# Optimization experiments

Measured on AMD Instinct MI355X. Metric: run time of the kernel, lower is better.

## Reference

```python
import jax, jax.numpy as jnp
import numpy as np

B, M = 1024, 200000
D_IN, DIM, D_OUT = 256, 128, 10
T = 1.0
EPS = 1e-7


def setup_inputs() -> dict:
    key = jax.random.key(0)
    k1, k2, k3, k4, k5 = jax.random.split(key, 5)
    x = jax.random.normal(k1, (B, D_IN), dtype=jnp.float32)
    y = jax.random.randint(k2, (B,), 0, D_OUT)
    candidate_x = jax.random.normal(k3, (M, D_IN), dtype=jnp.float32)
    candidate_y = jax.random.randint(k4, (M,), 0, D_OUT)
    W_enc = jax.random.normal(k5, (DIM, D_IN), dtype=jnp.float32) * (1.0 / np.sqrt(D_IN))
    b_enc = jnp.zeros((DIM,), dtype=jnp.float32)
    return {"x": x, "y": y, "candidate_x": candidate_x, "candidate_y": candidate_y,
            "W_enc": W_enc, "b_enc": b_enc, "is_train": 0}


def reference(x, y, candidate_x, candidate_y, W_enc, b_enc, is_train):
    # eval path (is_train == 0): no candidate subsampling, no diagonal masking
    h = x @ W_enc.T + b_enc            # [B, DIM]
    hc = candidate_x @ W_enc.T + b_enc  # [M, DIM]
    # pairwise L2 distance (cdist, p=2)
    sq = jnp.sum(h * h, axis=-1, keepdims=True) + jnp.sum(hc * hc, axis=-1)[None, :] \
         - 2.0 * (h @ hc.T)            # [B, M]
    dist = jnp.sqrt(jnp.maximum(sq, 0.0)) / T
    p = jax.nn.softmax(-dist, axis=-1)  # [B, M]
    y1h = jax.nn.one_hot(candidate_y, D_OUT, dtype=h.dtype)  # [M, D_OUT]
    logits = p @ y1h                    # [B, D_OUT]
    return jnp.log(logits + EPS)
```

## Files before the change

kernel.cpp:

```cpp
#include <hip/hip_runtime.h>
#include <hip/hip_bf16.h>
#include <math.h>

#define B_N   1024
#define M_N   200000
#define DIN   256
#define DIMN  128
#define DOUT  10
#define EPS_F 1e-7f
#define M_PAD 200064
#define NBY   1563
#define CTILES 8
#define NGRP  ((NBY + CTILES - 1)/CTILES)
#define YPAD  200

typedef __bf16 bf16_t;
typedef __bf16 bf16x8 __attribute__((ext_vector_type(8)));
typedef float  f32x4  __attribute__((ext_vector_type(4)));


__global__ void cvt_w_kernel(const float* __restrict__ W, bf16_t* __restrict__ Wb){
    int i = blockIdx.x*256 + threadIdx.x;
    if (i < DIMN*DIN) Wb[i] = (bf16_t)W[i];
}

__global__ void hist_kernel(const int* __restrict__ cy, int* __restrict__ hist){
    __shared__ int h[DOUT];
    if (threadIdx.x < DOUT) h[threadIdx.x] = 0;
    __syncthreads();
    for (int i = blockIdx.x*blockDim.x + threadIdx.x; i < M_N; i += gridDim.x*blockDim.x)
        atomicAdd(&h[cy[i]], 1);
    __syncthreads();
    if (threadIdx.x < DOUT) atomicAdd(&hist[threadIdx.x*16], h[threadIdx.x]);
}

__global__ void prefix_kernel(const int* __restrict__ hist, int* __restrict__ cs){
    if (threadIdx.x == 0 && blockIdx.x == 0){
        int acc = 0;
        for (int c = 0; c < DOUT; ++c){ cs[c] = acc; acc += hist[c*16]; }
        cs[DOUT] = acc;
    }
}


__global__ __launch_bounds__(256) void encode_kernel(
    const float* __restrict__ src, const bf16_t* __restrict__ Wb,
    bf16_t* __restrict__ out, float* __restrict__ onorm, int N,
    const int* __restrict__ ycls, int* __restrict__ counters,
    const int* __restrict__ cs)
{
    __shared__ bf16_t As[128][136];
    __shared__ int   posL[128];
    __shared__ float nbuf[128][2];
    __shared__ int   cntL[DOUT], baseL[DOUT];
    const int tid = threadIdx.x;
    const int r0  = blockIdx.x*128;

    int myc = -1, myrank = 0;
    if (ycls != nullptr){
        if (tid < DOUT) cntL[tid] = 0;
        __syncthreads();
        if (tid < 128 && r0 + tid < N){
            myc = ycls[r0 + tid];
            myrank = atomicAdd(&cntL[myc], 1);
        }
        __syncthreads();
        if (tid < DOUT && cntL[tid] > 0)
            baseL[tid] = atomicAdd(&counters[tid*16], cntL[tid]);
        __syncthreads();
    }
    if (tid < 128)
        posL[tid] = (myc >= 0) ? (cs[myc] + baseL[myc] + myrank) : (r0 + tid);

    const int lane = tid & 63, wid = tid >> 6;
    const int wr = wid >> 1, wc = wid & 1;
    const int l15 = lane & 15, quad = lane >> 4;
    const int cbase = wc*64;

    bf16x8 ball[2][4];
    #pragma unroll
    for (int kh = 0; kh < 2; ++kh)
        #pragma unroll
        for (int ks = 0; ks < 4; ++ks){
            ball[kh][ks] = *(const bf16x8*)(Wb + (size_t)(cbase + 0*16 + l15)*DIN + kh*128 + ks*32 + quad*8);
        }

    f32x4 acc[4][4] = {};
    #pragma unroll
    for (int kh = 0; kh < 2; ++kh){
        __syncthreads();
        #pragma unroll
        for (int i = 0; i < 8; ++i){
            int idx = i*256 + tid;
            int row = idx >> 4;
            int col = (idx & 15)*8;
            int rr  = r0 + row; if (rr > N-1) rr = N-1;
            const float4* p4 = (const float4*)(src + (size_t)rr*DIN + kh*128 + col);
            float4 f0 = p4[0], f1 = p4[1];
            bf16x8 v;
            v[0]=(bf16_t)f0.x; v[1]=(bf16_t)f0.y; v[2]=(bf16_t)f0.z; v[3]=(bf16_t)f0.w;
            v[4]=(bf16_t)f1.x; v[5]=(bf16_t)f1.y; v[6]=(bf16_t)f1.z; v[7]=(bf16_t)f1.w;
            *(bf16x8*)&As[row][col] = v;
        }
        __syncthreads();
        #pragma unroll
        for (int ks = 0; ks < 4; ++ks){
            const int k  = ks*32 + quad*8;
            const int kg = kh*128 + k;
            bf16x8 a[4], b[4];
            b[0] = ball[kh][ks];
            #pragma unroll
            for (int ct = 1; ct < 4; ++ct)
                b[ct] = *(const bf16x8*)(Wb + (size_t)(cbase + ct*16 + l15)*DIN + kg);
            #pragma unroll
            for (int rt = 0; rt < 4; ++rt)
                a[rt] = *(const bf16x8*)&As[wr*64 + rt*16 + l15][k];
            #pragma unroll
            for (int rt = 0; rt < 4; ++rt)
                #pragma unroll
                for (int ct = 0; ct < 4; ++ct)
                    acc[rt][ct] = __builtin_amdgcn_mfma_f32_16x16x32_bf16(a[rt], b[ct], acc[rt][ct], 0, 0, 0);
        }
    }

    float np[4][4];
    #pragma unroll
    for (int rt = 0; rt < 4; ++rt)
        #pragma unroll
        for (int r = 0; r < 4; ++r){
            float s = 0.f;
            #pragma unroll
            for (int ct = 0; ct < 4; ++ct){ float v = acc[rt][ct][r]; s += v*v; }
            np[rt][r] = s;
        }
    #pragma unroll
    for (int m = 1; m < 16; m <<= 1)
        #pragma unroll
        for (int rt = 0; rt < 4; ++rt)
            #pragma unroll
            for (int r = 0; r < 4; ++r)
                np[rt][r] += __shfl_xor(np[rt][r], m, 64);
    if (l15 == 0){
        #pragma unroll
        for (int rt = 0; rt < 4; ++rt)
            #pragma unroll
            for (int r = 0; r < 4; ++r)
                nbuf[wr*64 + rt*16 + quad*4 + r][wc] = np[rt][r];
    }

    __syncthreads();

    #pragma unroll
    for (int rt = 0; rt < 4; ++rt)
        #pragma unroll
        for (int r = 0; r < 4; ++r){
            int rl = wr*64 + rt*16 + quad*4 + r;
            #pragma unroll
            for (int ct = 0; ct < 4; ++ct)
                As[rl][cbase + ct*16 + l15] = (bf16_t)acc[rt][ct][r];
        }
    __syncthreads();

    {
        const int rsub = tid >> 4;
        const int cpos = (tid & 15)*8;
        #pragma unroll
        for (int p = 0; p < 8; ++p){
            int rl = p*16 + rsub;
            size_t rowp = (size_t)posL[rl]*DIMN;
            *(bf16x8*)(out + rowp + cpos) = *(const bf16x8*)&As[rl][cpos];
        }
    }
    if (tid < 128){
        int rs = r0 + tid;
        if (rs < N) onorm[posL[tid]] = nbuf[tid][0] + nbuf[tid][1];
    }
}


__device__ __forceinline__ void gld_lds16(const bf16_t* g, bf16_t* l){
    __builtin_amdgcn_global_load_lds((const __attribute__((address_space(1))) void*)g,
                                     (__attribute__((address_space(3))) void*)l, 16, 0, 0);
}

__device__ __forceinline__ void bfly16(float (&s)[2][4]){
    #pragma unroll
    for (int m = 1; m < 16; m <<= 1)
        #pragma unroll
        for (int rt = 0; rt < 2; ++rt)
            #pragma unroll
            for (int r = 0; r < 4; ++r)
                s[rt][r] += __shfl_xor(s[rt][r], m, 64);
}

__device__ __forceinline__ void flushC(float (&s)[2][4], int c, int rbase,
                                       int quad, int l15, float* __restrict__ accG){
    bfly16(s);
    if (l15 == 0){
        #pragma unroll
        for (int rt = 0; rt < 2; ++rt)
            #pragma unroll
            for (int r = 0; r < 4; ++r)
                atomicAdd(&accG[(size_t)(rbase + rt*16 + quad*4 + r)*16 + c], s[rt][r]);
    }
}

__global__ __launch_bounds__(512, 4) void fused_kernel(
    const bf16_t* __restrict__ hb, const bf16_t* __restrict__ hcb,
    const float* __restrict__ hn, const float* __restrict__ hcn,
    const int* __restrict__ csg, float* __restrict__ accG)
{
    const int lin = blockIdx.y*8 + blockIdx.x;
    const int i8  = lin & 7;
    const int t   = lin >> 3;
    const int q   = t >> 3;
    const int r8  = t & 7;
    const int bx  = r8;
    const int yg  = q*8 + i8;
    if (yg >= NGRP) return;

    __shared__ bf16_t Bs0[128][128];
    __shared__ bf16_t Bs1[128][128];
    const int tid = threadIdx.x;
    const int lane = tid & 63, wid = tid >> 6;
    const int wr = wid >> 1, wc = wid & 1;
    const int l15 = lane & 15, quad = lane >> 4;
    const int rbase = bx*128 + wr*32;

    bf16x8 a[4][2];
    #pragma unroll
    for (int ks = 0; ks < 4; ++ks)
        #pragma unroll
        for (int rt = 0; rt < 2; ++rt)
            a[ks][rt] = *(const bf16x8*)(hb + (size_t)(rbase + rt*16 + l15)*DIMN + ks*32 + quad*8);

    float hnv[2][4];
    #pragma unroll
    for (int rt = 0; rt < 2; ++rt)
        #pragma unroll
        for (int r = 0; r < 4; ++r)
            hnv[rt][r] = hn[rbase + rt*16 + quad*4 + r];

    int cseg[DOUT+1];
    #pragma unroll
    for (int i = 0; i <= DOUT; ++i) cseg[i] = __builtin_amdgcn_readfirstlane(csg[i]);

    const int by0 = yg*CTILES;
    int nt = NBY - by0; if (nt > CTILES) nt = CTILES;

    float s[2][4] = {};
    int curC = -1;

    auto stage = [&](bf16_t (&Bsb)[128][128], int by){
        const int cb = by*128;
        #pragma unroll
        for (int i = 0; i < 4; ++i){
            int c   = i*512 + tid;
            int col = c >> 4, j = c & 15;
            int cc  = cb + col; if (cc > M_N-1) cc = M_N-1;
            const bf16_t* g = hcb + (size_t)cc*DIMN + ((j ^ (col & 7)) << 3);
            bf16_t* l = &Bsb[0][0] + ((i*512 + (wid << 6)) << 3);
            gld_lds16(g, l);
        }
    };

    auto compute = [&](const bf16_t (&Bsb)[128][128], int by){
        const int cbase0 = by*128;
        f32x4 acc[2][4] = {};
        const char* bsb = (const char*)&Bsb[0][0];
        #pragma unroll
        for (int ks = 0; ks < 4; ++ks){
            bf16x8 b[4];
            #pragma unroll
            for (int ct = 0; ct < 4; ++ct){
                int row = wc*64 + ct*16 + l15;
                int off = (row << 8) + ((((ks << 6) + (quad << 4))) ^ ((l15 & 7) << 4));
                b[ct] = *(const bf16x8*)(bsb + off);
            }
            #pragma unroll
            for (int rt = 0; rt < 2; ++rt)
                #pragma unroll
                for (int ct = 0; ct < 4; ++ct)
                    acc[rt][ct] = __builtin_amdgcn_mfma_f32_16x16x32_bf16(a[ks][rt], b[ct], acc[rt][ct], 0, 0, 0);
        }

        float hcnv[4];
        #pragma unroll
        for (int ct = 0; ct < 4; ++ct){
            int cc = cbase0 + wc*64 + ct*16 + l15;
            hcnv[ct] = (cc < M_N) ? hcn[cc] : 1e30f;
        }
        #pragma unroll
        for (int rt = 0; rt < 2; ++rt)
            #pragma unroll
            for (int ct = 0; ct < 4; ++ct)
                #pragma unroll
                for (int r = 0; r < 4; ++r){
                    float sq = fmaxf(fmaf(-2.0f, acc[rt][ct][r], hnv[rt][r] + hcnv[ct]), 0.0f);
                    acc[rt][ct][r] = __expf(-__builtin_amdgcn_sqrtf(sq));
                }

        const int lastc = min(cbase0 + 127, M_N - 1);
        int cLo = 0, cHi = 0;
        #pragma unroll
        for (int c = 1; c < DOUT; ++c){
            if (cbase0 >= cseg[c]) cLo = c;
            if (lastc  >= cseg[c]) cHi = c;
        }

        if (cLo == curC && cHi == curC){
            #pragma unroll
            for (int rt = 0; rt < 2; ++rt)
                #pragma unroll
                for (int r = 0; r < 4; ++r){
                    float v0 = acc[rt][0][r] + acc[rt][1][r];
                    float v1 = acc[rt][2][r] + acc[rt][3][r];
                    s[rt][r] += v0 + v1;
                }
        } else {
            if (curC >= 0) flushC(s, curC, rbase, quad, l15, accG);
            #pragma unroll
            for (int rt = 0; rt < 2; ++rt)
                #pragma unroll
                for (int r = 0; r < 4; ++r) s[rt][r] = 0.f;
            for (int c = cLo; c <= cHi; ++c){
                const int s0 = cseg[c], s1 = cseg[c+1];
                float m[2][4];
                #pragma unroll
                for (int rt = 0; rt < 2; ++rt)
                    #pragma unroll
                    for (int r = 0; r < 4; ++r){
                        float v = 0.f;
                        #pragma unroll
                        for (int ct = 0; ct < 4; ++ct){
                            int cc = cbase0 + wc*64 + ct*16 + l15;
                            v += (cc >= s0 && cc < s1) ? acc[rt][ct][r] : 0.f;
                        }
                        m[rt][r] = v;
                    }
                if (c == cHi){
                    #pragma unroll
                    for (int rt = 0; rt < 2; ++rt)
                        #pragma unroll
                        for (int r = 0; r < 4; ++r) s[rt][r] = m[rt][r];
                    curC = cHi;
                } else {
                    flushC(m, c, rbase, quad, l15, accG);
                }
            }
        }
    };

    stage(Bs0, by0);
    __syncthreads();

    #pragma unroll 1
    for (int tp = 0; tp < CTILES/2; ++tp){
        int t0 = tp*2;
        if (t0 >= nt) break;
        if (t0 + 1 < nt) stage(Bs1, by0 + t0 + 1);
        compute(Bs0, by0 + t0);
        __syncthreads();
        int t1 = t0 + 1;
        if (t1 >= nt) break;
        if (t1 + 1 < nt) stage(Bs0, by0 + t1 + 1);
        compute(Bs1, by0 + t1);
        __syncthreads();
    }
    if (curC >= 0) flushC(s, curC, rbase, quad, l15, accG);
}

__global__ void finalize_kernel(const float* __restrict__ accG, float* __restrict__ out){
    int b = blockIdx.x*blockDim.x + threadIdx.x;
    if (b < B_N){
        float v[DOUT]; float den = 0.f;
        #pragma unroll
        for (int c = 0; c < DOUT; ++c){ v[c] = accG[b*16 + c]; den += v[c]; }
        float inv = (den > 0.f) ? 1.0f/den : 0.f;
        #pragma unroll
        for (int c = 0; c < DOUT; ++c) out[b*DOUT + c] = logf(v[c]*inv + EPS_F);
    }
}


extern "C" void kernel_launch(void* const* d_in, const int* in_sizes, int n_in,
                              void* d_out, int out_size, void* d_ws, size_t ws_size,
                              hipStream_t stream)
{
    const float* x  = (const float*)d_in[0];
    const float* cx = (const float*)d_in[2];
    const int*   cy = (const int*)d_in[3];
    const float* W  = (const float*)d_in[4];
    float* out = (float*)d_out;

    char* w = (char*)d_ws;
    size_t off = 0;
    bf16_t* hcb = (bf16_t*)(w + off); off += (size_t)M_PAD*DIMN*2;
    bf16_t* hb  = (bf16_t*)(w + off); off += (size_t)B_N*DIMN*2;
    float*  hcn = (float*) (w + off); off += (size_t)M_PAD*4;
    float*  hn  = (float*) (w + off); off += (size_t)B_N*4;
    bf16_t* Wb  = (bf16_t*)(w + off); off += (size_t)DIMN*DIN*2;
    size_t zoff = off;
    float* accG = (float*)(w + off); off += (size_t)B_N*16*4;
    int* hist     = (int*)(w + off); off += 16*DOUT*4;
    int* counters = (int*)(w + off); off += 16*DOUT*4;
    int* csg      = (int*)(w + off); off += 64;
    size_t zsize = off - zoff;

    hipMemsetAsync(w + zoff, 0, zsize, stream);
    cvt_w_kernel<<<dim3((DIMN*DIN + 255)/256), dim3(256), 0, stream>>>(W, Wb);
    hist_kernel<<<dim3(256), dim3(256), 0, stream>>>(cy, hist);
    prefix_kernel<<<dim3(1), dim3(1), 0, stream>>>(hist, csg);
    encode_kernel<<<dim3(M_PAD/128), dim3(256), 0, stream>>>(cx, Wb, hcb, hcn, M_N, cy, counters, csg);
    encode_kernel<<<dim3(B_N/128), dim3(256), 0, stream>>>(x, Wb, hb, hn, B_N, nullptr, nullptr, nullptr);
    fused_kernel<<<dim3(8, YPAD), dim3(512), 0, stream>>>(hb, hcb, hn, hcn, csg, accG);
    finalize_kernel<<<dim3((B_N + 255)/256), dim3(256), 0, stream>>>(accG, out);
}
```

Baseline: 482.4 us.

## Halve candidate tile, use exp2 with prescaled norms, merge encode launches

The fused distance/softmax kernel now stages 64-column candidate tiles instead of 128, with 16 tiles per group and a higher occupancy hint. Staging uses incrementing global pointers instead of recomputing addresses. The exp(-sqrt) is rewritten as a native exp2 with norms and the dot-product factor prescaled by log2(e)^2. Per-column-half accumulators are split into separate slots to reduce atomic contention, and finalize sums the two slots. The two encode launches are merged into one grid, which removes a launch but adds branching per block.

Result: slower. 607.3 us (+25.9%).

```diff
diff --git a/kernel.cpp b/kernel.cpp
--- a/kernel.cpp
+++ b/kernel.cpp
@@ -9,14 +9,26 @@
 #define DOUT  10
 #define EPS_F 1e-7f
 #define M_PAD 200064
-#define NBY   1563
-#define CTILES 8
-#define NGRP  ((NBY + CTILES - 1)/CTILES)
+#define MBLK  1563
+#define NBY64 3126
+#define TPG   16
+#define NGRP  ((NBY64 + TPG - 1)/TPG)
 #define YPAD  200
+#define L2E2  2.0813689810056077f
 
 typedef __bf16 bf16_t;
 typedef __bf16 bf16x8 __attribute__((ext_vector_type(8)));
 typedef float  f32x4  __attribute__((ext_vector_type(4)));
+
+__device__ __forceinline__ float fast_exp2(float x){
+#if __has_builtin(__builtin_amdgcn_exp2f)
+    return __builtin_amdgcn_exp2f(x);
+#else
+    float r;
+    asm("v_exp_f32 %0, %1" : "=v"(r) : "v"(x));
+    return r;
+#endif
+}
 
 
 __global__ void cvt_w_kernel(const float* __restrict__ W, bf16_t* __restrict__ Wb){
@@ -44,9 +56,11 @@
 
 
 __global__ __launch_bounds__(256) void encode_kernel(
-    const float* __restrict__ src, const bf16_t* __restrict__ Wb,
-    bf16_t* __restrict__ out, float* __restrict__ onorm, int N,
-    const int* __restrict__ ycls, int* __restrict__ counters,
+    const float* __restrict__ cx, const float* __restrict__ xb,
+    const bf16_t* __restrict__ Wb,
+    bf16_t* __restrict__ hcb, float* __restrict__ hcn,
+    bf16_t* __restrict__ hb,  float* __restrict__ hn,
+    const int* __restrict__ cy, int* __restrict__ counters,
     const int* __restrict__ cs)
 {
     __shared__ bf16_t As[128][136];
@@ -54,7 +68,13 @@
     __shared__ float nbuf[128][2];
     __shared__ int   cntL[DOUT], baseL[DOUT];
     const int tid = threadIdx.x;
-    const int r0  = blockIdx.x*128;
+
+    const float* src; bf16_t* out; float* onorm; int N; const int* ycls; int r0;
+    if ((int)blockIdx.x < MBLK){
+        src = cx; out = hcb; onorm = hcn; N = M_N; ycls = cy; r0 = blockIdx.x*128;
+    } else {
+        src = xb; out = hb;  onorm = hn;  N = B_N; ycls = nullptr; r0 = (blockIdx.x - MBLK)*128;
+    }
 
     int myc = -1, myrank = 0;
     if (ycls != nullptr){
@@ -81,9 +101,8 @@
     #pragma unroll
     for (int kh = 0; kh < 2; ++kh)
         #pragma unroll
-        for (int ks = 0; ks < 4; ++ks){
-            ball[kh][ks] = *(const bf16x8*)(Wb + (size_t)(cbase + 0*16 + l15)*DIN + kh*128 + ks*32 + quad*8);
-        }
+        for (int ks = 0; ks < 4; ++ks)
+            ball[kh][ks] = *(const bf16x8*)(Wb + (size_t)(cbase + l15)*DIN + kh*128 + ks*32 + quad*8);
 
     f32x4 acc[4][4] = {};
     #pragma unroll
@@ -194,18 +213,18 @@
 }
 
 __device__ __forceinline__ void flushC(float (&s)[2][4], int c, int rbase,
-                                       int quad, int l15, float* __restrict__ accG){
+                                       int quad, int l15, float* __restrict__ accGp){
     bfly16(s);
     if (l15 == 0){
         #pragma unroll
         for (int rt = 0; rt < 2; ++rt)
             #pragma unroll
             for (int r = 0; r < 4; ++r)
-                atomicAdd(&accG[(size_t)(rbase + rt*16 + quad*4 + r)*16 + c], s[rt][r]);
-    }
-}
-
-__global__ __launch_bounds__(512, 4) void fused_kernel(
+                atomicAdd(&accGp[(size_t)(rbase + rt*16 + quad*4 + r)*32 + c], s[rt][r]);
+    }
+}
+
+__global__ __launch_bounds__(512, 6) void fused_kernel(
     const bf16_t* __restrict__ hb, const bf16_t* __restrict__ hcb,
     const float* __restrict__ hn, const float* __restrict__ hcn,
     const int* __restrict__ csg, float* __restrict__ accG)
@@ -219,8 +238,8 @@
     const int yg  = q*8 + i8;
     if (yg >= NGRP) return;
 
-    __shared__ bf16_t Bs0[128][128];
-    __shared__ bf16_t Bs1[128][128];
+    __shared__ bf16_t Bs0[64][128];
+    __shared__ bf16_t Bs1[64][128];
     const int tid = threadIdx.x;
     const int lane = tid & 63, wid = tid >> 6;
     const int wr = wid >> 1, wc = wid & 1;
@@ -239,68 +258,69 @@
     for (int rt = 0; rt < 2; ++rt)
         #pragma unroll
         for (int r = 0; r < 4; ++r)
-            hnv[rt][r] = hn[rbase + rt*16 + quad*4 + r];
+            hnv[rt][r] = hn[rbase + rt*16 + quad*4 + r] * L2E2;
 
     int cseg[DOUT+1];
     #pragma unroll
     for (int i = 0; i <= DOUT; ++i) cseg[i] = __builtin_amdgcn_readfirstlane(csg[i]);
 
-    const int by0 = yg*CTILES;
-    int nt = NBY - by0; if (nt > CTILES) nt = CTILES;
-
+    const int by0 = yg*TPG;
+    int nt = NBY64 - by0; if (nt > TPG) nt = TPG;
+
+    float* accGp = accG + wc*16;
     float s[2][4] = {};
     int curC = -1;
 
-    auto stage = [&](bf16_t (&Bsb)[128][128], int by){
-        const int cb = by*128;
-        #pragma unroll
-        for (int i = 0; i < 4; ++i){
-            int c   = i*512 + tid;
-            int col = c >> 4, j = c & 15;
-            int cc  = cb + col; if (cc > M_N-1) cc = M_N-1;
-            const bf16_t* g = hcb + (size_t)cc*DIMN + ((j ^ (col & 7)) << 3);
-            bf16_t* l = &Bsb[0][0] + ((i*512 + (wid << 6)) << 3);
-            gld_lds16(g, l);
-        }
+    const int c1 = 512 + tid;
+    const int col0 = tid >> 4,  j0 = tid & 15;
+    const int col1 = c1  >> 4,  j1 = c1  & 15;
+    const bf16_t* gp0 = hcb + (size_t)(by0*64 + col0)*DIMN + ((j0 ^ (col0 & 7)) << 3);
+    const bf16_t* gp1 = hcb + (size_t)(by0*64 + col1)*DIMN + ((j1 ^ (col1 & 7)) << 3);
+
+    auto stage = [&](bf16_t* Bsb){
+        gld_lds16(gp0, Bsb + ((wid << 6) << 3));
+        gld_lds16(gp1, Bsb + ((512 + (wid << 6)) << 3));
+        gp0 += (size_t)64*DIMN;
+        gp1 += (size_t)64*DIMN;
     };
 
-    auto compute = [&](const bf16_t (&Bsb)[128][128], int by){
-        const int cbase0 = by*128;
-        f32x4 acc[2][4] = {};
-        const char* bsb = (const char*)&Bsb[0][0];
+    auto compute = [&](const bf16_t* Bsb, int by){
+        const int cbase0 = by*64;
+        f32x4 acc[2][2] = {};
+        const char* bsb = (const char*)Bsb;
         #pragma unroll
         for (int ks = 0; ks < 4; ++ks){
-            bf16x8 b[4];
-            #pragma unroll
-            for (int ct = 0; ct < 4; ++ct){
-                int row = wc*64 + ct*16 + l15;
+            bf16x8 b[2];
+            #pragma unroll
+            for (int ct = 0; ct < 2; ++ct){
+                int row = wc*32 + ct*16 + l15;
                 int off = (row << 8) + ((((ks << 6) + (quad << 4))) ^ ((l15 & 7) << 4));
                 b[ct] = *(const bf16x8*)(bsb + off);
             }
             #pragma unroll
             for (int rt = 0; rt < 2; ++rt)
                 #pragma unroll
-                for (int ct = 0; ct < 4; ++ct)
+                for (int ct = 0; ct < 2; ++ct)
                     acc[rt][ct] = __builtin_amdgcn_mfma_f32_16x16x32_bf16(a[ks][rt], b[ct], acc[rt][ct], 0, 0, 0);
         }
 
-        float hcnv[4];
-        #pragma unroll
-        for (int ct = 0; ct < 4; ++ct){
-            int cc = cbase0 + wc*64 + ct*16 + l15;
-            hcnv[ct] = (cc < M_N) ? hcn[cc] : 1e30f;
+        float hcnv[2];
+        #pragma unroll
+        for (int ct = 0; ct < 2; ++ct){
+            int cc = cbase0 + wc*32 + ct*16 + l15;
+            hcnv[ct] = (cc < M_N) ? hcn[cc] * L2E2 : 1e30f;
         }
         #pragma unroll
         for (int rt = 0; rt < 2; ++rt)
             #pragma unroll
-            for (int ct = 0; ct < 4; ++ct)
+            for (int ct = 0; ct < 2; ++ct)
                 #pragma unroll
                 for (int r = 0; r < 4; ++r){
-                    float sq = fmaxf(fmaf(-2.0f, acc[rt][ct][r], hnv[rt][r] + hcnv[ct]), 0.0f);
-                    acc[rt][ct][r] = __expf(-__builtin_amdgcn_sqrtf(sq));
+                    float sq = fmaxf(fmaf(-2.0f*L2E2, acc[rt][ct][r], hnv[rt][r] + hcnv[ct]), 0.0f);
+                    acc[rt][ct][r] = fast_exp2(-__builtin_amdgcn_sqrtf(sq));
                 }
 
-        const int lastc = min(cbase0 + 127, M_N - 1);
+        const int lastc = min(cbase0 + 63, M_N - 1);
         int cLo = 0, cHi = 0;
         #pragma unroll
         for (int c = 1; c < DOUT; ++c){
@@ -312,13 +332,10 @@
             #pragma unroll
             for (int rt = 0; rt < 2; ++rt)
                 #pragma unroll
-                for (int r = 0; r < 4; ++r){
-                    float v0 = acc[rt][0][r] + acc[rt][1][r];
-                    float v1 = acc[rt][2][r] + acc[rt][3][r];
-                    s[rt][r] += v0 + v1;
-                }
+                for (int r = 0; r < 4; ++r)
+                    s[rt][r] += acc[rt][0][r] + acc[rt][1][r];
         } else {
-            if (curC >= 0) flushC(s, curC, rbase, quad, l15, accG);
+            if (curC >= 0) flushC(s, curC, rbase, quad, l15, accGp);
             #pragma unroll
             for (int rt = 0; rt < 2; ++rt)
                 #pragma unroll
@@ -332,8 +349,8 @@
                     for (int r = 0; r < 4; ++r){
                         float v = 0.f;
                         #pragma unroll
-                        for (int ct = 0; ct < 4; ++ct){
-                            int cc = cbase0 + wc*64 + ct*16 + l15;
+                        for (int ct = 0; ct < 2; ++ct){
+                            int cc = cbase0 + wc*32 + ct*16 + l15;
                             v += (cc >= s0 && cc < s1) ? acc[rt][ct][r] : 0.f;
                         }
                         m[rt][r] = v;
@@ -345,29 +362,29 @@
                         for (int r = 0; r < 4; ++r) s[rt][r] = m[rt][r];
                     curC = cHi;
                 } else {
-                    flushC(m, c, rbase, quad, l15, accG);
+                    flushC(m, c, rbase, quad, l15, accGp);
                 }
             }
         }
     };
 
-    stage(Bs0, by0);
+    stage(&Bs0[0][0]);
     __syncthreads();
 
     #pragma unroll 1
-    for (int tp = 0; tp < CTILES/2; ++tp){
+    for (int tp = 0; tp < TPG/2; ++tp){
         int t0 = tp*2;
         if (t0 >= nt) break;
-        if (t0 + 1 < nt) stage(Bs1, by0 + t0 + 1);
-        compute(Bs0, by0 + t0);
+        if (t0 + 1 < nt) stage(&Bs1[0][0]);
+        compute(&Bs0[0][0], by0 + t0);
         __syncthreads();
         int t1 = t0 + 1;
         if (t1 >= nt) break;
-        if (t1 + 1 < nt) stage(Bs0, by0 + t1 + 1);
-        compute(Bs1, by0 + t1);
-        __syncthreads();
-    }
-    if (curC >= 0) flushC(s, curC, rbase, quad, l15, accG);
+        if (t1 + 1 < nt) stage(&Bs0[0][0]);
+        compute(&Bs1[0][0], by0 + t1);
+        __syncthreads();
+    }
+    if (curC >= 0) flushC(s, curC, rbase, quad, l15, accGp);
 }
 
 __global__ void finalize_kernel(const float* __restrict__ accG, float* __restrict__ out){
@@ -375,7 +392,10 @@
     if (b < B_N){
         float v[DOUT]; float den = 0.f;
         #pragma unroll
-        for (int c = 0; c < DOUT; ++c){ v[c] = accG[b*16 + c]; den += v[c]; }
+        for (int c = 0; c < DOUT; ++c){
+            v[c] = accG[b*32 + c] + accG[b*32 + 16 + c];
+            den += v[c];
+        }
         float inv = (den > 0.f) ? 1.0f/den : 0.f;
         #pragma unroll
         for (int c = 0; c < DOUT; ++c) out[b*DOUT + c] = logf(v[c]*inv + EPS_F);
@@ -401,7 +421,7 @@
     float*  hn  = (float*) (w + off); off += (size_t)B_N*4;
     bf16_t* Wb  = (bf16_t*)(w + off); off += (size_t)DIMN*DIN*2;
     size_t zoff = off;
-    float* accG = (float*)(w + off); off += (size_t)B_N*16*4;
+    float* accG = (float*)(w + off); off += (size_t)B_N*32*4;
     int* hist     = (int*)(w + off); off += 16*DOUT*4;
     int* counters = (int*)(w + off); off += 16*DOUT*4;
     int* csg      = (int*)(w + off); off += 64;
@@ -411,8 +431,8 @@
     cvt_w_kernel<<<dim3((DIMN*DIN + 255)/256), dim3(256), 0, stream>>>(W, Wb);
     hist_kernel<<<dim3(256), dim3(256), 0, stream>>>(cy, hist);
     prefix_kernel<<<dim3(1), dim3(1), 0, stream>>>(hist, csg);
-    encode_kernel<<<dim3(M_PAD/128), dim3(256), 0, stream>>>(cx, Wb, hcb, hcn, M_N, cy, counters, csg);
-    encode_kernel<<<dim3(B_N/128), dim3(256), 0, stream>>>(x, Wb, hb, hn, B_N, nullptr, nullptr, nullptr);
+    encode_kernel<<<dim3(MBLK + B_N/128), dim3(256), 0, stream>>>(
+        cx, x, Wb, hcb, hcn, hb, hn, cy, counters, csg);
     fused_kernel<<<dim3(8, YPAD), dim3(512), 0, stream>>>(hb, hcb, hn, hcn, csg, accG);
     finalize_kernel<<<dim3((B_N + 255)/256), dim3(256), 0, stream>>>(accG, out);
 }
```
